# Optimization experiments

Measured on AMD Instinct MI355X. Metric: run time of the kernel, lower is better.

Reference implementation:

```python
import jax, jax.numpy as jnp
import numpy as np

K = 3
STRIDE = 1
PAD = 1
DIL = 1


def _conv2d(x, w, b, stride, pad):
    y = jax.lax.conv_general_dilated(
        x, w, (stride, stride), [(pad, pad), (pad, pad)],
        dimension_numbers=('NCHW', 'OIHW', 'NCHW'))
    return y + b[None, :, None, None]


def setup_inputs() -> dict:
    key = jax.random.key(0)
    ks = jax.random.split(key, 6)
    N, Cin, Cout, H, W = 4, 64, 64, 128, 128
    x = jax.random.normal(ks[0], (N, Cin, H, W), jnp.float32)
    w_off = jax.random.normal(ks[1], (2 * K * K, Cin, K, K), jnp.float32) * 0.01
    b_off = jnp.zeros((2 * K * K,), jnp.float32)
    w_mask = jax.random.normal(ks[2], (K * K, Cin, K, K), jnp.float32) * 0.01
    b_mask = jnp.zeros((K * K,), jnp.float32)
    weight = jax.random.normal(ks[3], (Cout, Cin, K, K), jnp.float32) * 0.05
    bias = jax.random.normal(ks[4], (Cout,), jnp.float32)
    return {"x": x, "w_off": w_off, "b_off": b_off,
            "w_mask": w_mask, "b_mask": b_mask,
            "weight": weight, "bias": bias}


def _deform_conv(x, offset, weight, bias):
    # x: [N,C,H,W]; offset: [N,2*K2,Ho,Wo] with channel layout (dy,dx) per kernel pt
    N, C, H, W = x.shape
    K2 = K * K
    Ho, Wo = offset.shape[2], offset.shape[3]
    off_y = offset[:, 0::2]  # [N,K2,Ho,Wo]
    off_x = offset[:, 1::2]
    ki = jnp.arange(K2) // K
    kj = jnp.arange(K2) % K
    base_y = (jnp.arange(Ho) * STRIDE - PAD)[None, :, None] + (ki * DIL)[:, None, None]
    base_x = (jnp.arange(Wo) * STRIDE - PAD)[None, None, :] + (kj * DIL)[:, None, None]
    py = base_y[None].astype(off_y.dtype) + off_y  # [N,K2,Ho,Wo]
    px = base_x[None].astype(off_x.dtype) + off_x
    y0 = jnp.floor(py)
    x0 = jnp.floor(px)
    wy = py - y0
    wx = px - x0
    xf = x.reshape(N, C, H * W)

    def corner(yi, xi):
        valid = (yi >= 0) & (yi <= H - 1) & (xi >= 0) & (xi <= W - 1)
        yc = jnp.clip(yi, 0, H - 1).astype(jnp.int32)
        xc = jnp.clip(xi, 0, W - 1).astype(jnp.int32)
        idx = (yc * W + xc).reshape(N, -1)  # [N, K2*Ho*Wo]
        g = jnp.take_along_axis(xf, idx[:, None, :], axis=2)  # [N,C,K2*Ho*Wo]
        g = g.reshape(N, C, K2, Ho, Wo)
        return g * valid[:, None].astype(x.dtype)

    # bilinear interpolation with zero padding outside the image
    val = ((1 - wy) * (1 - wx))[:, None] * corner(y0, x0) \
        + ((1 - wy) * wx)[:, None] * corner(y0, x0 + 1) \
        + (wy * (1 - wx))[:, None] * corner(y0 + 1, x0) \
        + (wy * wx)[:, None] * corner(y0 + 1, x0 + 1)  # [N,C,K2,Ho,Wo]
    out = jnp.einsum('nckhw,ock->nohw', val,
                     weight.reshape(weight.shape[0], C, K2))
    return out + bias[None, :, None, None]


def reference(x, w_off, b_off, w_mask, b_mask, weight, bias):
    offset = _conv2d(x, w_off, b_off, STRIDE, PAD)              # [N,2*K2,Ho,Wo]
    mask = jax.nn.sigmoid(_conv2d(x, w_mask, b_mask, STRIDE, PAD))  # [N,K2,Ho,Wo]
    # source does mask.repeat(1,2,1,1) then offset*mask, then plain deform_conv2d
    offset = offset * jnp.concatenate([mask, mask], axis=1)
    return _deform_conv(x, offset, weight, bias)
```

## Files before the change

kernel.cpp:

```cpp
#include <hip/hip_runtime.h>
#include <math.h>

#define HD 128
#define WD 128
#define WP 130
#define CIN 64
#define COUT 64
#define NB 4
#define K2 9
#define HW (HD*WD)
#define CK 576
#define TP 32
#define TPF 16
#define NKK 18

#define WAM   (4 * NKK * 64 * 8)
#define WAO   (2 * NKK * 64 * 8)
#define XTP   ((size_t)NB * WP * WP * CIN)
#define OFFSZ ((size_t)NB * K2 * HW)
#define WTSZ  ((size_t)CK * COUT)

#define PRE_T 1024
#define PRE_H 65
#define PRE_P ((WAM + WAO) / 256)
#define HALO_PER_N 33024
#define HALO_W8 16512

typedef __attribute__((ext_vector_type(8))) short short8;
typedef __attribute__((ext_vector_type(4))) float f32x4;
typedef _Float16 half8 __attribute__((ext_vector_type(8)));
typedef _Float16 half2v __attribute__((ext_vector_type(2)));

__device__ inline unsigned short f2bf(float v) {
    unsigned int u = __float_as_uint(v);
    unsigned int r = u + 0x7fffu + ((u >> 16) & 1u);
    return (unsigned short)(r >> 16);
}
__device__ inline short f2h(float v) {
    _Float16 h = (_Float16)v;
    short s; __builtin_memcpy(&s, &h, 2); return s;
}
__device__ inline unsigned int pack_f16(float a, float b) {
    auto h = __builtin_amdgcn_cvt_pkrtz(a, b);
    unsigned int u; __builtin_memcpy(&u, &h, 4); return u;
}
__device__ inline half2v dup_h2(float a) {
    auto h = __builtin_amdgcn_cvt_pkrtz(a, a);
    half2v r; __builtin_memcpy(&r, &h, 4); return r;
}

__global__ __launch_bounds__(256) void pre_kernel(
    const float* __restrict__ x,
    const float* __restrict__ weight,
    const float* __restrict__ w_off,
    const float* __restrict__ w_mask,
    unsigned short* __restrict__ xp,
    short* __restrict__ mhi, short* __restrict__ ohi)
{
    __shared__ float tile[64][66];
    int bid = blockIdx.x;
    int t = threadIdx.x;

    if (bid < PRE_T) {
        int half = bid & 1;
        int h = (bid >> 1) & 127;
        int n = bid >> 8;
        int w0 = half * 64;
        int g = t >> 6, wl = t & 63;
        const float* xb = x + ((size_t)n * CIN) * HW + h * WD + w0;
        #pragma unroll
        for (int i = 0; i < 16; i++) {
            int cc = i * 4 + g;
            tile[wl][cc] = xb[(size_t)cc * HW + wl];
        }
        __syncthreads();
        size_t rowbase = (((size_t)n * WP + (h + 1)) * WP + (w0 + 1)) * CIN;
        #pragma unroll
        for (int i = 0; i < 8; i++) {
            int u = i * 256 + t;
            int ww = u >> 5;
            int cp = (u & 31) * 2;
            float2 v = *(const float2*)&tile[ww][cp];
            *(unsigned int*)&xp[rowbase + (size_t)ww * CIN + cp] = pack_f16(v.x, v.y);
        }
    } else if (bid < PRE_T + PRE_H) {
        int widx = (bid - PRE_T) * 256 + t;
        if (widx < HALO_W8) {
            int s = widx * 8;
            int n = s / HALO_PER_N;
            int v = s - n * HALO_PER_N;
            size_t nb = (size_t)n * WP * WP * CIN;
            size_t base;
            if (v < 8320) {
                base = nb + v;
            } else if (v < 16640) {
                base = nb + (size_t)129 * WP * CIN + (v - 8320);
            } else if (v < 24832) {
                int v2 = v - 16640; int h = 1 + (v2 >> 6); int c = v2 & 63;
                base = nb + (size_t)h * WP * CIN + c;
            } else {
                int v3 = v - 24832; int h = 1 + (v3 >> 6); int c = v3 & 63;
                base = nb + ((size_t)h * WP + 129) * CIN + c;
            }
            short8 z = {0, 0, 0, 0, 0, 0, 0, 0};
            *(short8*)&xp[base] = z;
        }
    } else {
        int gid = (bid - PRE_T - PRE_H) * 256 + t;
        if (gid < WAM) {
            int idx = gid;
            int jj = idx & 7;
            int lane = (idx >> 3) & 63;
            int kk = (idx >> 9) % NKK;
            int mt = (idx >> 9) / NKK;
            int o = mt * 16 + (lane & 15);
            int rp = kk * 32 + (lane >> 4) * 8 + jj;
            int k = rp >> 6, c = rp & 63;
            mhi[idx] = f2h(weight[((size_t)o * CIN + c) * 9 + k]);
        } else {
            int idx = gid - WAM;
            int jj = idx & 7;
            int lane = (idx >> 3) & 63;
            int kk = (idx >> 9) % NKK;
            int mt = (idx >> 9) / NKK;
            int j = mt * 16 + (lane & 15);
            int rp = kk * 32 + (lane >> 4) * 8 + jj;
            int k = rp >> 6, c = rp & 63;
            float w = 0.f;
            if (j < 18)      w = w_off[((size_t)j * CIN + c) * 9 + k];
            else if (j < 27) w = w_mask[((size_t)(j - 18) * CIN + c) * 9 + k];
            ohi[idx] = f2h(w);
        }
    }
}

__global__ __launch_bounds__(256, 4) void fused_kernel(
    const unsigned short* __restrict__ xp,
    const short* __restrict__ waM_hi,
    const short* __restrict__ waO_hi,
    const float* __restrict__ b_off, const float* __restrict__ b_mask,
    const float* __restrict__ bias,
    float* __restrict__ out)
{
    __shared__ __align__(16) short val_s[72 * 256];
    __shared__ __align__(16) float U[27 * 32];

    int t = threadIdx.x;
    int wv = t >> 6;
    int lane = t & 63;
    int wo0 = blockIdx.x * TP;
    int ho  = blockIdx.y;
    int n   = blockIdx.z;
    const unsigned short* xpn = xp + (size_t)n * WP * WP * CIN;
    int p16 = lane & 15, quad = lane >> 4;

    half8 apre[6];
    #pragma unroll
    for (int kk = 0; kk < 6; kk++)
        apre[kk] = *(const half8*)&waM_hi[((wv * NKK + kk) * 64 + lane) * 8];

    #pragma unroll
    for (int i = 0; i < 9; i++) {
        int u = t + 256 * i;
        int tap = u >> 8;
        int p = (u >> 3) & 31;
        int g = u & 7;
        int ti = tap / 3, tj = tap - ti * 3;
        const short8 v = *(const short8*)&xpn[((size_t)(ho + ti) * WP + (wo0 + p + tj)) * CIN + g * 8];
        int c2 = tap * 8 + g;
        *(short8*)&val_s[c2 * 256 + ((p + c2) & 31) * 8] = v;
    }
    __syncthreads();

    if (wv < 2) {
        int jt = wv;
        f32x4 c0a = {0.f, 0.f, 0.f, 0.f};
        f32x4 c1a = {0.f, 0.f, 0.f, 0.f};
        #pragma unroll
        for (int kk = 0; kk < NKK; kk++) {
            int abase = ((jt * NKK + kk) * 64 + lane) * 8;
            half8 ah = *(const half8*)&waO_hi[abase];
            int c2 = kk * 4 + quad;
            half8 b0 = *(const half8*)&val_s[c2 * 256 + ((p16 + c2) & 31) * 8];
            half8 b1 = *(const half8*)&val_s[c2 * 256 + ((16 + p16 + c2) & 31) * 8];
            c0a = __builtin_amdgcn_mfma_f32_16x16x32_f16(ah, b0, c0a, 0, 0, 0);
            c1a = __builtin_amdgcn_mfma_f32_16x16x32_f16(ah, b1, c1a, 0, 0, 0);
        }
        #pragma unroll
        for (int i = 0; i < 4; i++) {
            int j = jt * 16 + quad * 4 + i;
            if (j < 27) {
                float bv = (j < 18) ? b_off[j] : b_mask[j - 18];
                U[j * 32 + p16] = c0a[i] + bv;
                U[j * 32 + 16 + p16] = c1a[i] + bv;
            }
        }
    }
    __syncthreads();

    float rwy[2], rwx[2];
    unsigned int rmeta[2];
    #pragma unroll
    for (int pass = 0; pass < 2; pass++) {
        int u = t + pass * 256;
        if (u < K2 * TP) {
            int k = u >> 5, p = u & 31;
            float oy_raw = U[(2 * k) * 32 + p];
            float ox_raw = U[(2 * k + 1) * 32 + p];
            float my = 1.f / (1.f + expf(-U[(18 + (2 * k) % 9) * 32 + p]));
            float mx = 1.f / (1.f + expf(-U[(18 + (2 * k + 1) % 9) * 32 + p]));
            float oy = oy_raw * my;
            float ox = ox_raw * mx;
            int ki = k / 3, kj = k - ki * 3;
            int wo = wo0 + p;
            float py = (float)(ho - 1 + ki) + oy;
            float px = (float)(wo - 1 + kj) + ox;
            float y0f = floorf(py), x0f = floorf(px);
            float wy = py - y0f, wx = px - x0f;
            int y0 = (int)y0f, x0 = (int)x0f;
            int y0c = min(max(y0, 0), HD - 1);
            int y1c = min(max(y0 + 1, 0), HD - 1);
            int x0c = min(max(x0, 0), WD - 1);
            int x1c = min(max(x0 + 1, 0), WD - 1);
            bool vy0 = (y0 >= 0) && (y0 < HD);
            bool vy1 = (y0 + 1 >= 0) && (y0 + 1 < HD);
            bool vx0 = (x0 >= 0) && (x0 < WD);
            bool vx1 = (x0 + 1 >= 0) && (x0 + 1 < WD);
            unsigned int cvA = (vy0 && vx0) ? 1u : 0u;
            unsigned int cvB = (vy0 && vx1) ? 1u : 0u;
            unsigned int cvC = (vy1 && vx0) ? 1u : 0u;
            unsigned int cvD = (vy1 && vx1) ? 1u : 0u;
            rwy[pass] = wy;
            rwx[pass] = wx;
            rmeta[pass] = (unsigned int)y0c | ((unsigned int)x0c << 7)
                        | ((unsigned int)(y1c - y0c) << 14) | ((unsigned int)(x1c - x0c) << 15)
                        | (cvA << 16) | (cvB << 17) | (cvC << 18) | (cvD << 19);
        }
    }
    __syncthreads();
    #pragma unroll
    for (int pass = 0; pass < 2; pass++) {
        int u = t + pass * 256;
        if (u < K2 * TP) {
            U[u] = rwy[pass];
            U[288 + u] = rwx[pass];
            ((unsigned int*)U)[576 + u] = rmeta[pass];
        }
    }
    __syncthreads();

    #pragma unroll
    for (int i = 0; i < 9; i++) {
        int u = t + 256 * i;
        int task = u >> 3;
        int g = u & 7;
        int c0 = g * 8;
        int k = task >> 5, p = task & 31;
        float wy = U[task];
        float wx = U[288 + task];
        unsigned int m = ((const unsigned int*)U)[576 + task];
        float wy0 = 1.f - wy, wx0 = 1.f - wx;
        float wA = (m & 0x10000u) ? wy0 * wx0 : 0.f;
        float wB = (m & 0x20000u) ? wy0 * wx  : 0.f;
        float wC = (m & 0x40000u) ? wy  * wx0 : 0.f;
        float wD = (m & 0x80000u) ? wy  * wx  : 0.f;
        half2v wa2 = dup_h2(wA), wb2 = dup_h2(wB), wc2 = dup_h2(wC), wd2 = dup_h2(wD);
        int y0c = (int)(m & 127u);
        int x0c = (int)((m >> 7) & 127u);
        int ry0 = (y0c + 1) * (WP * CIN);
        int ry1 = ry0 + (int)((m >> 14) & 1u) * (WP * CIN);
        int cx0 = (x0c + 1) * CIN + c0;
        int cx1 = (x0c + 1) * CIN + (int)((m >> 15) & 1u) * CIN + c0;
        uint4 qa = *(const uint4*)&xpn[ry0 + cx0];
        uint4 qb = *(const uint4*)&xpn[ry0 + cx1];
        uint4 qc = *(const uint4*)&xpn[ry1 + cx0];
        uint4 qd = *(const uint4*)&xpn[ry1 + cx1];
        unsigned int qa_[4] = {qa.x, qa.y, qa.z, qa.w};
        unsigned int qb_[4] = {qb.x, qb.y, qb.z, qb.w};
        unsigned int qc_[4] = {qc.x, qc.y, qc.z, qc.w};
        unsigned int qd_[4] = {qd.x, qd.y, qd.z, qd.w};
        unsigned int r_[4];
        #pragma unroll
        for (int d = 0; d < 4; d++) {
            half2v ha, hb, hc, hd;
            __builtin_memcpy(&ha, &qa_[d], 4);
            __builtin_memcpy(&hb, &qb_[d], 4);
            __builtin_memcpy(&hc, &qc_[d], 4);
            __builtin_memcpy(&hd, &qd_[d], 4);
            half2v gg = wa2 * ha + wb2 * hb + wc2 * hc + wd2 * hd;
            __builtin_memcpy(&r_[d], &gg, 4);
        }
        uint4 r = {r_[0], r_[1], r_[2], r_[3]};
        int c2 = k * 8 + g;
        *(uint4*)&val_s[c2 * 256 + ((p + c2) & 31) * 8] = r;
    }
    __syncthreads();

    f32x4 a0 = {0.f, 0.f, 0.f, 0.f};
    f32x4 a1 = {0.f, 0.f, 0.f, 0.f};
    #pragma unroll
    for (int kk = 0; kk < NKK; kk++) {
        half8 ah;
        if (kk < 6) ah = apre[kk];
        else        ah = *(const half8*)&waM_hi[((wv * NKK + kk) * 64 + lane) * 8];
        int c2 = kk * 4 + quad;
        half8 b0 = *(const half8*)&val_s[c2 * 256 + ((p16 + c2) & 31) * 8];
        half8 b1 = *(const half8*)&val_s[c2 * 256 + ((16 + p16 + c2) & 31) * 8];
        a0 = __builtin_amdgcn_mfma_f32_16x16x32_f16(ah, b0, a0, 0, 0, 0);
        a1 = __builtin_amdgcn_mfma_f32_16x16x32_f16(ah, b1, a1, 0, 0, 0);
    }

    size_t obase = ((size_t)n * COUT) * HW + (size_t)ho * WD + wo0;
    #pragma unroll
    for (int i = 0; i < 4; i++) {
        int o = wv * 16 + quad * 4 + i;
        float bv = bias[o];
        out[obase + (size_t)o * HW + p16] = a0[i] + bv;
        out[obase + (size_t)o * HW + 16 + p16] = a1[i] + bv;
    }
}

__global__ void transpose_w_kernel(const float* __restrict__ w, float* __restrict__ wt) {
    int i = blockIdx.x * 256 + threadIdx.x;
    int o = i / CK;
    int ck = i - o * CK;
    wt[ck * COUT + o] = w[i];
}

__global__ __launch_bounds__(256) void offmask_kernel(
    const float* __restrict__ x,
    const float* __restrict__ w_off, const float* __restrict__ b_off,
    const float* __restrict__ w_mask, const float* __restrict__ b_mask,
    float* __restrict__ offy, float* __restrict__ offx)
{
    __shared__ float ws[CK][27];
    int t = threadIdx.x;
    for (int i = t; i < CK * 27; i += 256) {
        int j = i % 27;
        int citap = i / 27;
        int ci = citap / 9;
        int tap = citap - ci * 9;
        float v;
        if (j < 18) v = w_off[(j * CIN + ci) * 9 + tap];
        else        v = w_mask[((j - 18) * CIN + ci) * 9 + tap];
        ws[citap][j] = v;
    }
    __syncthreads();

    int pix = blockIdx.x * 256 + t;
    int n  = pix >> 14;
    int ho = (pix >> 7) & 127;
    int wo = pix & 127;

    float acc[27];
    #pragma unroll
    for (int j = 0; j < 18; j++) acc[j] = b_off[j];
    #pragma unroll
    for (int j = 0; j < 9; j++)  acc[18 + j] = b_mask[j];

    int offs[9];
    bool oks[9];
    #pragma unroll
    for (int dy = 0; dy < 3; dy++) {
        int y = ho - 1 + dy;
        #pragma unroll
        for (int dx = 0; dx < 3; dx++) {
            int xx = wo - 1 + dx;
            bool ok = (y >= 0) && (y < HD) && (xx >= 0) && (xx < WD);
            oks[dy * 3 + dx] = ok;
            offs[dy * 3 + dx] = (ok ? y : 0) * WD + (ok ? xx : 0);
        }
    }
    const float* xn = x + (size_t)n * CIN * HW;
    for (int ci = 0; ci < CIN; ci++) {
        const float* xc = xn + (size_t)ci * HW;
        float v[9];
        #pragma unroll
        for (int tap = 0; tap < 9; tap++)
            v[tap] = oks[tap] ? xc[offs[tap]] : 0.f;
        #pragma unroll
        for (int tap = 0; tap < 9; tap++) {
            const float* wrow = ws[ci * 9 + tap];
            float vv = v[tap];
            #pragma unroll
            for (int j = 0; j < 27; j++) acc[j] += wrow[j] * vv;
        }
    }
    float m[9];
    #pragma unroll
    for (int j = 0; j < 9; j++) m[j] = 1.f / (1.f + expf(-acc[18 + j]));
    #pragma unroll
    for (int k = 0; k < 9; k++) {
        int cy = 2 * k, cx = 2 * k + 1;
        float my = m[cy < 9 ? cy : cy - 9];
        float mx = m[cx < 9 ? cx : cx - 9];
        size_t o = (((size_t)n * K2 + k) * HD + ho) * WD + wo;
        offy[o] = acc[cy] * my;
        offx[o] = acc[cx] * mx;
    }
}

__global__ __launch_bounds__(256) void deform_kernel(
    const float* __restrict__ x,
    const float* __restrict__ offy, const float* __restrict__ offx,
    const float* __restrict__ wt,
    const float* __restrict__ bias,
    float* __restrict__ out)
{
    __shared__ __align__(16) float val_f[CK * TPF];
    __shared__ float4 p_w4[K2 * TPF];
    __shared__ int4   p_idx4[K2 * TPF];

    int t = threadIdx.x;
    int wo0 = blockIdx.x * TPF;
    int ho  = blockIdx.y;
    int n   = blockIdx.z;

    if (t < K2 * TPF) {
        int k = t >> 4, p = t & 15;
        int wo = wo0 + p;
        size_t oi = (((size_t)n * K2 + k) * HD + ho) * WD + wo;
        float oy = offy[oi], ox = offx[oi];
        int ki = k / 3, kj = k - ki * 3;
        float py = (float)(ho - 1 + ki) + oy;
        float px = (float)(wo - 1 + kj) + ox;
        float y0f = floorf(py), x0f = floorf(px);
        float wy = py - y0f, wx = px - x0f;
        int y0 = (int)y0f, x0 = (int)x0f;
        float wy0 = 1.f - wy, wx0 = 1.f - wx;
        int y0c = min(max(y0, 0), HD - 1);
        int y1c = min(max(y0 + 1, 0), HD - 1);
        int x0c = min(max(x0, 0), WD - 1);
        int x1c = min(max(x0 + 1, 0), WD - 1);
        bool vy0 = (y0 >= 0) && (y0 < HD);
        bool vy1 = (y0 + 1 >= 0) && (y0 + 1 < HD);
        bool vx0 = (x0 >= 0) && (x0 < WD);
        bool vx1 = (x0 + 1 >= 0) && (x0 + 1 < WD);
        float4 w4;
        w4.x = (vy0 && vx0) ? wy0 * wx0 : 0.f;
        w4.y = (vy0 && vx1) ? wy0 * wx  : 0.f;
        w4.z = (vy1 && vx0) ? wy  * wx0 : 0.f;
        w4.w = (vy1 && vx1) ? wy  * wx  : 0.f;
        int4 i4;
        i4.x = y0c * WD + x0c;
        i4.y = y0c * WD + x1c;
        i4.z = y1c * WD + x0c;
        i4.w = y1c * WD + x1c;
        p_w4[t] = w4;
        p_idx4[t] = i4;
    }
    __syncthreads();

    const float* xn = x + (size_t)n * CIN * HW;
    for (int e = t; e < CK * TPF; e += 256) {
        int row = e >> 4, p = e & 15;
        int cc = row / 9, k = row - cc * 9;
        int task = (k << 4) | p;
        float4 w4 = p_w4[task];
        int4  i4 = p_idx4[task];
        const float* xc = xn + (size_t)cc * HW;
        val_f[e] = w4.x * xc[i4.x] + w4.y * xc[i4.y]
                 + w4.z * xc[i4.z] + w4.w * xc[i4.w];
    }
    __syncthreads();

    int o = t & 63, q = t >> 6;
    float4 acc = {0.f, 0.f, 0.f, 0.f};
    const float4* v4 = (const float4*)val_f;
    const float* wp = wt + o;
    #pragma unroll 4
    for (int r = 0; r < CK; r++) {
        float w = wp[r * COUT];
        float4 vv = v4[r * 4 + q];
        acc.x += w * vv.x; acc.y += w * vv.y;
        acc.z += w * vv.z; acc.w += w * vv.w;
    }
    float b = bias[o];
    acc.x += b; acc.y += b; acc.z += b; acc.w += b;
    __syncthreads();
    float4* o4 = (float4*)val_f;
    o4[o * 4 + q] = acc;
    __syncthreads();
    size_t obase = ((size_t)n * COUT) * HW + (size_t)ho * WD + wo0;
    #pragma unroll
    for (int i = 0; i < 4; i++) {
        int l = t + 256 * i;
        int oo = l >> 4, p = l & 15;
        out[obase + (size_t)oo * HW + p] = val_f[l];
    }
}

extern "C" void kernel_launch(void* const* d_in, const int* in_sizes, int n_in,
                              void* d_out, int out_size, void* d_ws, size_t ws_size,
                              hipStream_t stream) {
    const float* x      = (const float*)d_in[0];
    const float* w_off  = (const float*)d_in[1];
    const float* b_off  = (const float*)d_in[2];
    const float* w_mask = (const float*)d_in[3];
    const float* b_mask = (const float*)d_in[4];
    const float* weight = (const float*)d_in[5];
    const float* bias   = (const float*)d_in[6];
    float* out = (float*)d_out;

    short* base = (short*)d_ws;
    short* waM_hi = base;
    short* waO_hi = waM_hi + WAM;
    unsigned short* xp = (unsigned short*)(waO_hi + WAO);
    size_t need = ((size_t)WAM + WAO + XTP) * sizeof(short);

    if (ws_size >= need) {
        pre_kernel<<<PRE_T + PRE_H + PRE_P, 256, 0, stream>>>(
            x, weight, w_off, w_mask, xp, waM_hi, waO_hi);
        fused_kernel<<<dim3(WD / TP, HD, NB), 256, 0, stream>>>(
            xp, waM_hi, waO_hi, b_off, b_mask, bias, out);
    } else {
        float* offy = (float*)d_ws;
        float* offx = offy + OFFSZ;
        float* wt   = offx + OFFSZ;
        transpose_w_kernel<<<144, 256, 0, stream>>>(weight, wt);
        offmask_kernel<<<256, 256, 0, stream>>>(x, w_off, b_off, w_mask, b_mask, offy, offx);
        deform_kernel<<<dim3(WD / TPF, HD, NB), 256, 0, stream>>>(x, offy, offx, wt, bias, out);
    }
}
```

Baseline: 107.9 us.

## Compute sampling metadata in registers and distribute via wave shuffles

```diff
diff --git a/kernel.cpp b/kernel.cpp
--- a/kernel.cpp
+++ b/kernel.cpp
@@ -13,6 +13,7 @@
 #define TP 32
 #define TPF 16
 #define NKK 18
+#define US 33
 
 #define WAM   (4 * NKK * 64 * 8)
 #define WAO   (2 * NKK * 64 * 8)
@@ -134,6 +135,35 @@
     }
 }
 
+#define CALC_TRIPLE(kk_, owy, owx, ometa) { \
+    const int k_ = (kk_); \
+    float oy_raw = U[(2 * k_) * US + p]; \
+    float ox_raw = U[(2 * k_ + 1) * US + p]; \
+    float my = 1.f / (1.f + expf(-U[(18 + (2 * k_) % 9) * US + p])); \
+    float mx = 1.f / (1.f + expf(-U[(18 + (2 * k_ + 1) % 9) * US + p])); \
+    float oy = oy_raw * my; \
+    float ox = ox_raw * mx; \
+    const int ki_ = k_ / 3, kj_ = k_ - ki_ * 3; \
+    float py = (float)(ho - 1 + ki_) + oy; \
+    float px = (float)(wo0 + p - 1 + kj_) + ox; \
+    float y0f = floorf(py), x0f = floorf(px); \
+    float wy_ = py - y0f, wx_ = px - x0f; \
+    int y0 = (int)y0f, x0 = (int)x0f; \
+    int y0c = min(max(y0, 0), HD - 1); \
+    int y1c = min(max(y0 + 1, 0), HD - 1); \
+    int x0c = min(max(x0, 0), WD - 1); \
+    int x1c = min(max(x0 + 1, 0), WD - 1); \
+    bool vy0 = (y0 >= 0) && (y0 < HD); \
+    bool vy1 = (y0 + 1 >= 0) && (y0 + 1 < HD); \
+    bool vx0 = (x0 >= 0) && (x0 < WD); \
+    bool vx1 = (x0 + 1 >= 0) && (x0 + 1 < WD); \
+    owy = wy_; owx = wx_; \
+    ometa = (unsigned int)y0c | ((unsigned int)x0c << 7) \
+          | ((unsigned int)(y1c - y0c) << 14) | ((unsigned int)(x1c - x0c) << 15) \
+          | ((vy0 && vx0) ? 0x10000u : 0u) | ((vy0 && vx1) ? 0x20000u : 0u) \
+          | ((vy1 && vx0) ? 0x40000u : 0u) | ((vy1 && vx1) ? 0x80000u : 0u); \
+}
+
 __global__ __launch_bounds__(256, 4) void fused_kernel(
     const unsigned short* __restrict__ xp,
     const short* __restrict__ waM_hi,
@@ -143,7 +173,7 @@
     float* __restrict__ out)
 {
     __shared__ __align__(16) short val_s[72 * 256];
-    __shared__ __align__(16) float U[27 * 32];
+    __shared__ __align__(16) float U[27 * US];
 
     int t = threadIdx.x;
     int wv = t >> 6;
@@ -191,108 +221,66 @@
             int j = jt * 16 + quad * 4 + i;
             if (j < 27) {
                 float bv = (j < 18) ? b_off[j] : b_mask[j - 18];
-                U[j * 32 + p16] = c0a[i] + bv;
-                U[j * 32 + 16 + p16] = c1a[i] + bv;
+                U[j * US + p16] = c0a[i] + bv;
+                U[j * US + 16 + p16] = c1a[i] + bv;
             }
         }
     }
     __syncthreads();
 
-    float rwy[2], rwx[2];
-    unsigned int rmeta[2];
-    #pragma unroll
-    for (int pass = 0; pass < 2; pass++) {
-        int u = t + pass * 256;
-        if (u < K2 * TP) {
-            int k = u >> 5, p = u & 31;
-            float oy_raw = U[(2 * k) * 32 + p];
-            float ox_raw = U[(2 * k + 1) * 32 + p];
-            float my = 1.f / (1.f + expf(-U[(18 + (2 * k) % 9) * 32 + p]));
-            float mx = 1.f / (1.f + expf(-U[(18 + (2 * k + 1) % 9) * 32 + p]));
-            float oy = oy_raw * my;
-            float ox = ox_raw * mx;
-            int ki = k / 3, kj = k - ki * 3;
-            int wo = wo0 + p;
-            float py = (float)(ho - 1 + ki) + oy;
-            float px = (float)(wo - 1 + kj) + ox;
-            float y0f = floorf(py), x0f = floorf(px);
-            float wy = py - y0f, wx = px - x0f;
-            int y0 = (int)y0f, x0 = (int)x0f;
-            int y0c = min(max(y0, 0), HD - 1);
-            int y1c = min(max(y0 + 1, 0), HD - 1);
-            int x0c = min(max(x0, 0), WD - 1);
-            int x1c = min(max(x0 + 1, 0), WD - 1);
-            bool vy0 = (y0 >= 0) && (y0 < HD);
-            bool vy1 = (y0 + 1 >= 0) && (y0 + 1 < HD);
-            bool vx0 = (x0 >= 0) && (x0 < WD);
-            bool vx1 = (x0 + 1 >= 0) && (x0 + 1 < WD);
-            unsigned int cvA = (vy0 && vx0) ? 1u : 0u;
-            unsigned int cvB = (vy0 && vx1) ? 1u : 0u;
-            unsigned int cvC = (vy1 && vx0) ? 1u : 0u;
-            unsigned int cvD = (vy1 && vx1) ? 1u : 0u;
-            rwy[pass] = wy;
-            rwx[pass] = wx;
-            rmeta[pass] = (unsigned int)y0c | ((unsigned int)x0c << 7)
-                        | ((unsigned int)(y1c - y0c) << 14) | ((unsigned int)(x1c - x0c) << 15)
-                        | (cvA << 16) | (cvB << 17) | (cvC << 18) | (cvD << 19);
-        }
-    }
-    __syncthreads();
-    #pragma unroll
-    for (int pass = 0; pass < 2; pass++) {
-        int u = t + pass * 256;
-        if (u < K2 * TP) {
-            U[u] = rwy[pass];
-            U[288 + u] = rwx[pass];
-            ((unsigned int*)U)[576 + u] = rmeta[pass];
-        }
-    }
-    __syncthreads();
-
-    #pragma unroll
-    for (int i = 0; i < 9; i++) {
-        int u = t + 256 * i;
-        int task = u >> 3;
-        int g = u & 7;
-        int c0 = g * 8;
-        int k = task >> 5, p = task & 31;
-        float wy = U[task];
-        float wx = U[288 + task];
-        unsigned int m = ((const unsigned int*)U)[576 + task];
-        float wy0 = 1.f - wy, wx0 = 1.f - wx;
-        float wA = (m & 0x10000u) ? wy0 * wx0 : 0.f;
-        float wB = (m & 0x20000u) ? wy0 * wx  : 0.f;
-        float wC = (m & 0x40000u) ? wy  * wx0 : 0.f;
-        float wD = (m & 0x80000u) ? wy  * wx  : 0.f;
-        half2v wa2 = dup_h2(wA), wb2 = dup_h2(wB), wc2 = dup_h2(wC), wd2 = dup_h2(wD);
-        int y0c = (int)(m & 127u);
-        int x0c = (int)((m >> 7) & 127u);
-        int ry0 = (y0c + 1) * (WP * CIN);
-        int ry1 = ry0 + (int)((m >> 14) & 1u) * (WP * CIN);
-        int cx0 = (x0c + 1) * CIN + c0;
-        int cx1 = (x0c + 1) * CIN + (int)((m >> 15) & 1u) * CIN + c0;
-        uint4 qa = *(const uint4*)&xpn[ry0 + cx0];
-        uint4 qb = *(const uint4*)&xpn[ry0 + cx1];
-        uint4 qc = *(const uint4*)&xpn[ry1 + cx0];
-        uint4 qd = *(const uint4*)&xpn[ry1 + cx1];
-        unsigned int qa_[4] = {qa.x, qa.y, qa.z, qa.w};
-        unsigned int qb_[4] = {qb.x, qb.y, qb.z, qb.w};
-        unsigned int qc_[4] = {qc.x, qc.y, qc.z, qc.w};
-        unsigned int qd_[4] = {qd.x, qd.y, qd.z, qd.w};
-        unsigned int r_[4];
-        #pragma unroll
-        for (int d = 0; d < 4; d++) {
-            half2v ha, hb, hc, hd;
-            __builtin_memcpy(&ha, &qa_[d], 4);
-            __builtin_memcpy(&hb, &qb_[d], 4);
-            __builtin_memcpy(&hc, &qc_[d], 4);
-            __builtin_memcpy(&hd, &qd_[d], 4);
-            half2v gg = wa2 * ha + wb2 * hb + wc2 * hc + wd2 * hd;
-            __builtin_memcpy(&r_[d], &gg, 4);
-        }
-        uint4 r = {r_[0], r_[1], r_[2], r_[3]};
-        int c2 = k * 8 + g;
-        *(uint4*)&val_s[c2 * 256 + ((p + c2) & 31) * 8] = r;
+    {
+        int p = t >> 3, g = t & 7, c0 = g * 8;
+        float myWy, myWx; unsigned int myMeta;
+        CALC_TRIPLE(g, myWy, myWx, myMeta);
+        float w8y, w8x; unsigned int m8;
+        CALC_TRIPLE(8, w8y, w8x, m8);
+
+        #pragma unroll
+        for (int k = 0; k < 9; k++) {
+            float wy, wx; unsigned int m;
+            if (k < 8) {
+                int sl = (lane & 56) | k;
+                wy = __shfl(myWy, sl);
+                wx = __shfl(myWx, sl);
+                m  = (unsigned int)__shfl((int)myMeta, sl);
+            } else {
+                wy = w8y; wx = w8x; m = m8;
+            }
+            float wy0 = 1.f - wy, wx0 = 1.f - wx;
+            float wA = (m & 0x10000u) ? wy0 * wx0 : 0.f;
+            float wB = (m & 0x20000u) ? wy0 * wx  : 0.f;
+            float wC = (m & 0x40000u) ? wy  * wx0 : 0.f;
+            float wD = (m & 0x80000u) ? wy  * wx  : 0.f;
+            half2v wa2 = dup_h2(wA), wb2 = dup_h2(wB), wc2 = dup_h2(wC), wd2 = dup_h2(wD);
+            int y0c = (int)(m & 127u);
+            int x0c = (int)((m >> 7) & 127u);
+            int ry0 = (y0c + 1) * (WP * CIN);
+            int ry1 = ry0 + (int)((m >> 14) & 1u) * (WP * CIN);
+            int cx0 = (x0c + 1) * CIN + c0;
+            int cx1 = (x0c + 1) * CIN + (int)((m >> 15) & 1u) * CIN + c0;
+            uint4 qa = *(const uint4*)&xpn[ry0 + cx0];
+            uint4 qb = *(const uint4*)&xpn[ry0 + cx1];
+            uint4 qc = *(const uint4*)&xpn[ry1 + cx0];
+            uint4 qd = *(const uint4*)&xpn[ry1 + cx1];
+            unsigned int qa_[4] = {qa.x, qa.y, qa.z, qa.w};
+            unsigned int qb_[4] = {qb.x, qb.y, qb.z, qb.w};
+            unsigned int qc_[4] = {qc.x, qc.y, qc.z, qc.w};
+            unsigned int qd_[4] = {qd.x, qd.y, qd.z, qd.w};
+            unsigned int r_[4];
+            #pragma unroll
+            for (int d = 0; d < 4; d++) {
+                half2v ha, hb, hc, hd;
+                __builtin_memcpy(&ha, &qa_[d], 4);
+                __builtin_memcpy(&hb, &qb_[d], 4);
+                __builtin_memcpy(&hc, &qc_[d], 4);
+                __builtin_memcpy(&hd, &qd_[d], 4);
+                half2v gg = wa2 * ha + wb2 * hb + wc2 * hc + wd2 * hd;
+                __builtin_memcpy(&r_[d], &gg, 4);
+            }
+            uint4 r = {r_[0], r_[1], r_[2], r_[3]};
+            int c2 = k * 8 + g;
+            *(uint4*)&val_s[c2 * 256 + ((p + c2) & 31) * 8] = r;
+        }
     }
     __syncthreads();
 
```

Result: slower. 124.8 us (+15.6%).

## Move offset/mask conv into pre-kernel, pass bilinear metadata through workspace

Applied to the files above, without the earlier changes.

```diff
diff --git a/kernel.cpp b/kernel.cpp
--- a/kernel.cpp
+++ b/kernel.cpp
@@ -15,14 +15,14 @@
 #define NKK 18
 
 #define WAM   (4 * NKK * 64 * 8)
-#define WAO   (2 * NKK * 64 * 8)
 #define XTP   ((size_t)NB * WP * WP * CIN)
 #define OFFSZ ((size_t)NB * K2 * HW)
 #define WTSZ  ((size_t)CK * COUT)
 
 #define PRE_T 1024
 #define PRE_H 65
-#define PRE_P ((WAM + WAO) / 256)
+#define PRE_W 144
+#define PRE_C 256
 #define HALO_PER_N 33024
 #define HALO_W8 16512
 
@@ -31,11 +31,6 @@
 typedef _Float16 half8 __attribute__((ext_vector_type(8)));
 typedef _Float16 half2v __attribute__((ext_vector_type(2)));
 
-__device__ inline unsigned short f2bf(float v) {
-    unsigned int u = __float_as_uint(v);
-    unsigned int r = u + 0x7fffu + ((u >> 16) & 1u);
-    return (unsigned short)(r >> 16);
-}
 __device__ inline short f2h(float v) {
     _Float16 h = (_Float16)v;
     short s; __builtin_memcpy(&s, &h, 2); return s;
@@ -52,16 +47,19 @@
 __global__ __launch_bounds__(256) void pre_kernel(
     const float* __restrict__ x,
     const float* __restrict__ weight,
-    const float* __restrict__ w_off,
-    const float* __restrict__ w_mask,
+    const float* __restrict__ w_off, const float* __restrict__ b_off,
+    const float* __restrict__ w_mask, const float* __restrict__ b_mask,
     unsigned short* __restrict__ xp,
-    short* __restrict__ mhi, short* __restrict__ ohi)
+    short* __restrict__ mhi,
+    float* __restrict__ wyP, float* __restrict__ wxP,
+    unsigned int* __restrict__ metaP)
 {
-    __shared__ float tile[64][66];
+    __shared__ __align__(16) unsigned char smem[32256];
     int bid = blockIdx.x;
     int t = threadIdx.x;
 
     if (bid < PRE_T) {
+        float (*tile)[66] = (float (*)[66])smem;
         int half = bid & 1;
         int h = (bid >> 1) & 127;
         int n = bid >> 8;
@@ -105,114 +103,99 @@
             short8 z = {0, 0, 0, 0, 0, 0, 0, 0};
             *(short8*)&xp[base] = z;
         }
+    } else if (bid < PRE_T + PRE_H + PRE_W) {
+        int idx = (bid - PRE_T - PRE_H) * 256 + t;
+        int jj = idx & 7;
+        int lane = (idx >> 3) & 63;
+        int kk = (idx >> 9) % NKK;
+        int mt = (idx >> 9) / NKK;
+        int o = mt * 16 + (lane & 15);
+        int rp = kk * 32 + (lane >> 4) * 8 + jj;
+        int k = rp >> 6, c = rp & 63;
+        mhi[idx] = f2h(weight[((size_t)o * CIN + c) * 9 + k]);
     } else {
-        int gid = (bid - PRE_T - PRE_H) * 256 + t;
-        if (gid < WAM) {
-            int idx = gid;
-            int jj = idx & 7;
-            int lane = (idx >> 3) & 63;
-            int kk = (idx >> 9) % NKK;
-            int mt = (idx >> 9) / NKK;
-            int o = mt * 16 + (lane & 15);
-            int rp = kk * 32 + (lane >> 4) * 8 + jj;
-            int k = rp >> 6, c = rp & 63;
-            mhi[idx] = f2h(weight[((size_t)o * CIN + c) * 9 + k]);
-        } else {
-            int idx = gid - WAM;
-            int jj = idx & 7;
-            int lane = (idx >> 3) & 63;
-            int kk = (idx >> 9) % NKK;
-            int mt = (idx >> 9) / NKK;
-            int j = mt * 16 + (lane & 15);
-            int rp = kk * 32 + (lane >> 4) * 8 + jj;
-            int k = rp >> 6, c = rp & 63;
-            float w = 0.f;
-            if (j < 18)      w = w_off[((size_t)j * CIN + c) * 9 + k];
-            else if (j < 27) w = w_mask[((size_t)(j - 18) * CIN + c) * 9 + k];
-            ohi[idx] = f2h(w);
-        }
-    }
-}
-
-__global__ __launch_bounds__(256, 4) void fused_kernel(
-    const unsigned short* __restrict__ xp,
-    const short* __restrict__ waM_hi,
-    const short* __restrict__ waO_hi,
-    const float* __restrict__ b_off, const float* __restrict__ b_mask,
-    const float* __restrict__ bias,
-    float* __restrict__ out)
-{
-    __shared__ __align__(16) short val_s[72 * 256];
-    __shared__ __align__(16) float U[27 * 32];
-
-    int t = threadIdx.x;
-    int wv = t >> 6;
-    int lane = t & 63;
-    int wo0 = blockIdx.x * TP;
-    int ho  = blockIdx.y;
-    int n   = blockIdx.z;
-    const unsigned short* xpn = xp + (size_t)n * WP * WP * CIN;
-    int p16 = lane & 15, quad = lane >> 4;
-
-    half8 apre[6];
-    #pragma unroll
-    for (int kk = 0; kk < 6; kk++)
-        apre[kk] = *(const half8*)&waM_hi[((wv * NKK + kk) * 64 + lane) * 8];
-
-    #pragma unroll
-    for (int i = 0; i < 9; i++) {
-        int u = t + 256 * i;
-        int tap = u >> 8;
-        int p = (u >> 3) & 31;
-        int g = u & 7;
-        int ti = tap / 3, tj = tap - ti * 3;
-        const short8 v = *(const short8*)&xpn[((size_t)(ho + ti) * WP + (wo0 + p + tj)) * CIN + g * 8];
-        int c2 = tap * 8 + g;
-        *(short8*)&val_s[c2 * 256 + ((p + c2) & 31) * 8] = v;
-    }
-    __syncthreads();
-
-    if (wv < 2) {
-        int jt = wv;
-        f32x4 c0a = {0.f, 0.f, 0.f, 0.f};
-        f32x4 c1a = {0.f, 0.f, 0.f, 0.f};
-        #pragma unroll
-        for (int kk = 0; kk < NKK; kk++) {
-            int abase = ((jt * NKK + kk) * 64 + lane) * 8;
-            half8 ah = *(const half8*)&waO_hi[abase];
-            int c2 = kk * 4 + quad;
-            half8 b0 = *(const half8*)&val_s[c2 * 256 + ((p16 + c2) & 31) * 8];
-            half8 b1 = *(const half8*)&val_s[c2 * 256 + ((16 + p16 + c2) & 31) * 8];
-            c0a = __builtin_amdgcn_mfma_f32_16x16x32_f16(ah, b0, c0a, 0, 0, 0);
-            c1a = __builtin_amdgcn_mfma_f32_16x16x32_f16(ah, b1, c1a, 0, 0, 0);
-        }
-        #pragma unroll
-        for (int i = 0; i < 4; i++) {
-            int j = jt * 16 + quad * 4 + i;
-            if (j < 27) {
-                float bv = (j < 18) ? b_off[j] : b_mask[j - 18];
-                U[j * 32 + p16] = c0a[i] + bv;
-                U[j * 32 + 16 + p16] = c1a[i] + bv;
+        unsigned int (*wsH)[14] = (unsigned int (*)[14])smem;
+        for (int e = t; e < CK * 14; e += 256) {
+            int m = e % 14;
+            int citap = e / 14;
+            int ci = citap / 9, tap = citap - ci * 9;
+            int j0 = 2 * m, j1 = 2 * m + 1;
+            float w0 = (j0 < 18) ? w_off[((size_t)j0 * CIN + ci) * 9 + tap]
+                                 : w_mask[((size_t)(j0 - 18) * CIN + ci) * 9 + tap];
+            float w1;
+            if (j1 < 18)      w1 = w_off[((size_t)j1 * CIN + ci) * 9 + tap];
+            else if (j1 < 27) w1 = w_mask[((size_t)(j1 - 18) * CIN + ci) * 9 + tap];
+            else              w1 = 0.f;
+            wsH[citap][m] = pack_f16(w0, w1);
+        }
+        __syncthreads();
+
+        int pix = (bid - (PRE_T + PRE_H + PRE_W)) * 256 + t;
+        int n  = pix >> 14;
+        int ho = (pix >> 7) & 127;
+        int wo = pix & 127;
+
+        int offs[9];
+        bool oks[9];
+        #pragma unroll
+        for (int dy = 0; dy < 3; dy++) {
+            int y = ho - 1 + dy;
+            #pragma unroll
+            for (int dx = 0; dx < 3; dx++) {
+                int xx = wo - 1 + dx;
+                bool ok = (y >= 0) && (y < HD) && (xx >= 0) && (xx < WD);
+                oks[dy * 3 + dx] = ok;
+                offs[dy * 3 + dx] = (ok ? y : 0) * WD + (ok ? xx : 0);
             }
         }
-    }
-    __syncthreads();
-
-    float rwy[2], rwx[2];
-    unsigned int rmeta[2];
-    #pragma unroll
-    for (int pass = 0; pass < 2; pass++) {
-        int u = t + pass * 256;
-        if (u < K2 * TP) {
-            int k = u >> 5, p = u & 31;
-            float oy_raw = U[(2 * k) * 32 + p];
-            float ox_raw = U[(2 * k + 1) * 32 + p];
-            float my = 1.f / (1.f + expf(-U[(18 + (2 * k) % 9) * 32 + p]));
-            float mx = 1.f / (1.f + expf(-U[(18 + (2 * k + 1) % 9) * 32 + p]));
-            float oy = oy_raw * my;
-            float ox = ox_raw * mx;
+
+        float accf[27];
+        #pragma unroll
+        for (int j = 0; j < 27; j++) accf[j] = 0.f;
+
+        const float* xn = x + (size_t)n * CIN * HW;
+        #pragma unroll 1
+        for (int cc = 0; cc < 4; cc++) {
+            half2v acc2[14];
+            #pragma unroll
+            for (int m = 0; m < 14; m++) acc2[m] = (half2v)(_Float16)0.f;
+            for (int ci = cc * 16; ci < cc * 16 + 16; ci++) {
+                const float* xc = xn + (size_t)ci * HW;
+                float v[9];
+                #pragma unroll
+                for (int tap = 0; tap < 9; tap++)
+                    v[tap] = oks[tap] ? xc[offs[tap]] : 0.f;
+                #pragma unroll
+                for (int tap = 0; tap < 9; tap++) {
+                    half2v vh = dup_h2(v[tap]);
+                    const unsigned int* wrow = wsH[ci * 9 + tap];
+                    #pragma unroll
+                    for (int m = 0; m < 14; m++) {
+                        half2v w; __builtin_memcpy(&w, &wrow[m], 4);
+                        acc2[m] = vh * w + acc2[m];
+                    }
+                }
+            }
+            #pragma unroll
+            for (int m = 0; m < 14; m++) {
+                accf[2 * m] += (float)acc2[m][0];
+                if (2 * m + 1 < 27) accf[2 * m + 1] += (float)acc2[m][1];
+            }
+        }
+        #pragma unroll
+        for (int j = 0; j < 18; j++) accf[j] += b_off[j];
+        #pragma unroll
+        for (int j = 0; j < 9; j++)  accf[18 + j] += b_mask[j];
+
+        float mk[9];
+        #pragma unroll
+        for (int j = 0; j < 9; j++) mk[j] = 1.f / (1.f + expf(-accf[18 + j]));
+
+        #pragma unroll
+        for (int k = 0; k < 9; k++) {
+            float oy = accf[2 * k] * mk[(2 * k) % 9];
+            float ox = accf[2 * k + 1] * mk[(2 * k + 1) % 9];
             int ki = k / 3, kj = k - ki * 3;
-            int wo = wo0 + p;
             float py = (float)(ho - 1 + ki) + oy;
             float px = (float)(wo - 1 + kj) + ox;
             float y0f = floorf(py), x0f = floorf(px);
@@ -226,73 +209,86 @@
             bool vy1 = (y0 + 1 >= 0) && (y0 + 1 < HD);
             bool vx0 = (x0 >= 0) && (x0 < WD);
             bool vx1 = (x0 + 1 >= 0) && (x0 + 1 < WD);
-            unsigned int cvA = (vy0 && vx0) ? 1u : 0u;
-            unsigned int cvB = (vy0 && vx1) ? 1u : 0u;
-            unsigned int cvC = (vy1 && vx0) ? 1u : 0u;
-            unsigned int cvD = (vy1 && vx1) ? 1u : 0u;
-            rwy[pass] = wy;
-            rwx[pass] = wx;
-            rmeta[pass] = (unsigned int)y0c | ((unsigned int)x0c << 7)
-                        | ((unsigned int)(y1c - y0c) << 14) | ((unsigned int)(x1c - x0c) << 15)
-                        | (cvA << 16) | (cvB << 17) | (cvC << 18) | (cvD << 19);
-        }
-    }
-    __syncthreads();
-    #pragma unroll
-    for (int pass = 0; pass < 2; pass++) {
-        int u = t + pass * 256;
-        if (u < K2 * TP) {
-            U[u] = rwy[pass];
-            U[288 + u] = rwx[pass];
-            ((unsigned int*)U)[576 + u] = rmeta[pass];
-        }
-    }
-    __syncthreads();
-
-    #pragma unroll
-    for (int i = 0; i < 9; i++) {
-        int u = t + 256 * i;
-        int task = u >> 3;
-        int g = u & 7;
-        int c0 = g * 8;
-        int k = task >> 5, p = task & 31;
-        float wy = U[task];
-        float wx = U[288 + task];
-        unsigned int m = ((const unsigned int*)U)[576 + task];
-        float wy0 = 1.f - wy, wx0 = 1.f - wx;
-        float wA = (m & 0x10000u) ? wy0 * wx0 : 0.f;
-        float wB = (m & 0x20000u) ? wy0 * wx  : 0.f;
-        float wC = (m & 0x40000u) ? wy  * wx0 : 0.f;
-        float wD = (m & 0x80000u) ? wy  * wx  : 0.f;
-        half2v wa2 = dup_h2(wA), wb2 = dup_h2(wB), wc2 = dup_h2(wC), wd2 = dup_h2(wD);
-        int y0c = (int)(m & 127u);
-        int x0c = (int)((m >> 7) & 127u);
-        int ry0 = (y0c + 1) * (WP * CIN);
-        int ry1 = ry0 + (int)((m >> 14) & 1u) * (WP * CIN);
-        int cx0 = (x0c + 1) * CIN + c0;
-        int cx1 = (x0c + 1) * CIN + (int)((m >> 15) & 1u) * CIN + c0;
-        uint4 qa = *(const uint4*)&xpn[ry0 + cx0];
-        uint4 qb = *(const uint4*)&xpn[ry0 + cx1];
-        uint4 qc = *(const uint4*)&xpn[ry1 + cx0];
-        uint4 qd = *(const uint4*)&xpn[ry1 + cx1];
-        unsigned int qa_[4] = {qa.x, qa.y, qa.z, qa.w};
-        unsigned int qb_[4] = {qb.x, qb.y, qb.z, qb.w};
-        unsigned int qc_[4] = {qc.x, qc.y, qc.z, qc.w};
-        unsigned int qd_[4] = {qd.x, qd.y, qd.z, qd.w};
-        unsigned int r_[4];
-        #pragma unroll
-        for (int d = 0; d < 4; d++) {
-            half2v ha, hb, hc, hd;
-            __builtin_memcpy(&ha, &qa_[d], 4);
-            __builtin_memcpy(&hb, &qb_[d], 4);
-            __builtin_memcpy(&hc, &qc_[d], 4);
-            __builtin_memcpy(&hd, &qd_[d], 4);
-            half2v gg = wa2 * ha + wb2 * hb + wc2 * hc + wd2 * hd;
-            __builtin_memcpy(&r_[d], &gg, 4);
-        }
-        uint4 r = {r_[0], r_[1], r_[2], r_[3]};
-        int c2 = k * 8 + g;
-        *(uint4*)&val_s[c2 * 256 + ((p + c2) & 31) * 8] = r;
+            unsigned int meta = (unsigned int)y0c | ((unsigned int)x0c << 7)
+                | ((unsigned int)(y1c - y0c) << 14) | ((unsigned int)(x1c - x0c) << 15)
+                | ((vy0 && vx0) ? 0x10000u : 0u) | ((vy0 && vx1) ? 0x20000u : 0u)
+                | ((vy1 && vx0) ? 0x40000u : 0u) | ((vy1 && vx1) ? 0x80000u : 0u);
+            size_t pi = (size_t)(n * K2 + k) * HW + ho * WD + wo;
+            wyP[pi] = wy;
+            wxP[pi] = wx;
+            metaP[pi] = meta;
+        }
+    }
+}
+
+__global__ __launch_bounds__(256, 4) void fused_kernel(
+    const unsigned short* __restrict__ xp,
+    const short* __restrict__ waM_hi,
+    const float* __restrict__ wyP, const float* __restrict__ wxP,
+    const unsigned int* __restrict__ metaP,
+    const float* __restrict__ bias,
+    float* __restrict__ out)
+{
+    __shared__ __align__(16) short val_s[72 * 256];
+
+    int t = threadIdx.x;
+    int wv = t >> 6;
+    int lane = t & 63;
+    int wo0 = blockIdx.x * TP;
+    int ho  = blockIdx.y;
+    int n   = blockIdx.z;
+    const unsigned short* xpn = xp + (size_t)n * WP * WP * CIN;
+    int p16 = lane & 15, quad = lane >> 4;
+
+    half8 apre[8];
+    #pragma unroll
+    for (int kk = 0; kk < 8; kk++)
+        apre[kk] = *(const half8*)&waM_hi[((wv * NKK + kk) * 64 + lane) * 8];
+
+    {
+        int p = t >> 3, g = t & 7, c0 = g * 8;
+        size_t pbase = (size_t)(n * K2) * HW + (size_t)ho * WD + wo0 + p;
+        #pragma unroll
+        for (int i = 0; i < 9; i++) {
+            size_t pi = pbase + (size_t)i * HW;
+            float wy = wyP[pi];
+            float wx = wxP[pi];
+            unsigned int m = metaP[pi];
+            float wy0 = 1.f - wy, wx0 = 1.f - wx;
+            float wA = (m & 0x10000u) ? wy0 * wx0 : 0.f;
+            float wB = (m & 0x20000u) ? wy0 * wx  : 0.f;
+            float wC = (m & 0x40000u) ? wy  * wx0 : 0.f;
+            float wD = (m & 0x80000u) ? wy  * wx  : 0.f;
+            half2v wa2 = dup_h2(wA), wb2 = dup_h2(wB), wc2 = dup_h2(wC), wd2 = dup_h2(wD);
+            int y0c = (int)(m & 127u);
+            int x0c = (int)((m >> 7) & 127u);
+            int ry0 = (y0c + 1) * (WP * CIN);
+            int ry1 = ry0 + (int)((m >> 14) & 1u) * (WP * CIN);
+            int cx0 = (x0c + 1) * CIN + c0;
+            int cx1 = (x0c + 1) * CIN + (int)((m >> 15) & 1u) * CIN + c0;
+            uint4 qa = *(const uint4*)&xpn[ry0 + cx0];
+            uint4 qb = *(const uint4*)&xpn[ry0 + cx1];
+            uint4 qc = *(const uint4*)&xpn[ry1 + cx0];
+            uint4 qd = *(const uint4*)&xpn[ry1 + cx1];
+            unsigned int qa_[4] = {qa.x, qa.y, qa.z, qa.w};
+            unsigned int qb_[4] = {qb.x, qb.y, qb.z, qb.w};
+            unsigned int qc_[4] = {qc.x, qc.y, qc.z, qc.w};
+            unsigned int qd_[4] = {qd.x, qd.y, qd.z, qd.w};
+            unsigned int r_[4];
+            #pragma unroll
+            for (int d = 0; d < 4; d++) {
+                half2v ha, hb, hc, hd;
+                __builtin_memcpy(&ha, &qa_[d], 4);
+                __builtin_memcpy(&hb, &qb_[d], 4);
+                __builtin_memcpy(&hc, &qc_[d], 4);
+                __builtin_memcpy(&hd, &qd_[d], 4);
+                half2v gg = wa2 * ha + wb2 * hb + wc2 * hc + wd2 * hd;
+                __builtin_memcpy(&r_[d], &gg, 4);
+            }
+            uint4 r = {r_[0], r_[1], r_[2], r_[3]};
+            int c2 = i * 8 + g;
+            *(uint4*)&val_s[c2 * 256 + ((p + c2) & 31) * 8] = r;
+        }
     }
     __syncthreads();
 
@@ -301,7 +297,7 @@
     #pragma unroll
     for (int kk = 0; kk < NKK; kk++) {
         half8 ah;
-        if (kk < 6) ah = apre[kk];
+        if (kk < 8) ah = apre[kk];
         else        ah = *(const half8*)&waM_hi[((wv * NKK + kk) * 64 + lane) * 8];
         int c2 = kk * 4 + quad;
         half8 b0 = *(const half8*)&val_s[c2 * 256 + ((p16 + c2) & 31) * 8];
@@ -502,17 +498,18 @@
     const float* bias   = (const float*)d_in[6];
     float* out = (float*)d_out;
 
-    short* base = (short*)d_ws;
-    short* waM_hi = base;
-    short* waO_hi = waM_hi + WAM;
-    unsigned short* xp = (unsigned short*)(waO_hi + WAO);
-    size_t need = ((size_t)WAM + WAO + XTP) * sizeof(short);
+    short* waM_hi = (short*)d_ws;
+    unsigned short* xp = (unsigned short*)(waM_hi + WAM);
+    float* wyP = (float*)(xp + XTP);
+    float* wxP = wyP + OFFSZ;
+    unsigned int* metaP = (unsigned int*)(wxP + OFFSZ);
+    size_t need = (size_t)WAM * 2 + XTP * 2 + OFFSZ * 12;
 
     if (ws_size >= need) {
-        pre_kernel<<<PRE_T + PRE_H + PRE_P, 256, 0, stream>>>(
-            x, weight, w_off, w_mask, xp, waM_hi, waO_hi);
+        pre_kernel<<<PRE_T + PRE_H + PRE_W + PRE_C, 256, 0, stream>>>(
+            x, weight, w_off, b_off, w_mask, b_mask, xp, waM_hi, wyP, wxP, metaP);
         fused_kernel<<<dim3(WD / TP, HD, NB), 256, 0, stream>>>(
-            xp, waM_hi, waO_hi, b_off, b_mask, bias, out);
+            xp, waM_hi, wyP, wxP, metaP, bias, out);
     } else {
         float* offy = (float*)d_ws;
         float* offx = offy + OFFSZ;
```

New measurement: 191.4 us. 1.77x slower.

## Stage padded input window in LDS and gather bilinear corners from it

Applied to the files above, without the earlier changes.

```diff
diff --git a/kernel.cpp b/kernel.cpp
--- a/kernel.cpp
+++ b/kernel.cpp
@@ -13,6 +13,8 @@
 #define TP 32
 #define TPF 16
 #define NKK 18
+#define WR 6
+#define WC 36
 
 #define WAM   (4 * NKK * 64 * 8)
 #define WAO   (2 * NKK * 64 * 8)
@@ -31,11 +33,6 @@
 typedef _Float16 half8 __attribute__((ext_vector_type(8)));
 typedef _Float16 half2v __attribute__((ext_vector_type(2)));
 
-__device__ inline unsigned short f2bf(float v) {
-    unsigned int u = __float_as_uint(v);
-    unsigned int r = u + 0x7fffu + ((u >> 16) & 1u);
-    return (unsigned short)(r >> 16);
-}
 __device__ inline short f2h(float v) {
     _Float16 h = (_Float16)v;
     short s; __builtin_memcpy(&s, &h, 2); return s;
@@ -134,7 +131,9 @@
     }
 }
 
-__global__ __launch_bounds__(256, 4) void fused_kernel(
+#define WIN_ADDR(r, c, g) ((((r) * WC + (c)) * 8 + (((g) + (c)) & 7)) * 8)
+
+__global__ __launch_bounds__(256, 2) void fused_kernel(
     const unsigned short* __restrict__ xp,
     const short* __restrict__ waM_hi,
     const short* __restrict__ waO_hi,
@@ -142,6 +141,7 @@
     const float* __restrict__ bias,
     float* __restrict__ out)
 {
+    __shared__ __align__(16) short win_s[WR * WC * 64];
     __shared__ __align__(16) short val_s[72 * 256];
     __shared__ __align__(16) float U[27 * 32];
 
@@ -160,15 +160,16 @@
         apre[kk] = *(const half8*)&waM_hi[((wv * NKK + kk) * 64 + lane) * 8];
 
     #pragma unroll
-    for (int i = 0; i < 9; i++) {
+    for (int i = 0; i < 7; i++) {
         int u = t + 256 * i;
-        int tap = u >> 8;
-        int p = (u >> 3) & 31;
-        int g = u & 7;
-        int ti = tap / 3, tj = tap - ti * 3;
-        const short8 v = *(const short8*)&xpn[((size_t)(ho + ti) * WP + (wo0 + p + tj)) * CIN + g * 8];
-        int c2 = tap * 8 + g;
-        *(short8*)&val_s[c2 * 256 + ((p + c2) & 31) * 8] = v;
+        if (u < WR * WC * 8) {
+            int s = u >> 3, g = u & 7;
+            int r = s / WC, c = s - r * WC;
+            int yr = min(max(ho - 1 + r, 0), 129);
+            int xc = min(max(wo0 - 1 + c, 0), 129);
+            const short8 v = *(const short8*)&xpn[((size_t)yr * WP + xc) * CIN + g * 8];
+            *(short8*)&win_s[WIN_ADDR(r, c, g)] = v;
+        }
     }
     __syncthreads();
 
@@ -180,9 +181,15 @@
         for (int kk = 0; kk < NKK; kk++) {
             int abase = ((jt * NKK + kk) * 64 + lane) * 8;
             half8 ah = *(const half8*)&waO_hi[abase];
-            int c2 = kk * 4 + quad;
-            half8 b0 = *(const half8*)&val_s[c2 * 256 + ((p16 + c2) & 31) * 8];
-            half8 b1 = *(const half8*)&val_s[c2 * 256 + ((16 + p16 + c2) & 31) * 8];
+            const int tap = kk >> 1;
+            const int ti = tap / 3;
+            const int tj = tap - ti * 3;
+            int gg = (kk & 1) * 4 + quad;
+            int r = ti + 1;
+            int ca = p16 + tj + 1;
+            int cb = 16 + p16 + tj + 1;
+            half8 b0 = *(const half8*)&win_s[WIN_ADDR(r, ca, gg)];
+            half8 b1 = *(const half8*)&win_s[WIN_ADDR(r, cb, gg)];
             c0a = __builtin_amdgcn_mfma_f32_16x16x32_f16(ah, b0, c0a, 0, 0, 0);
             c1a = __builtin_amdgcn_mfma_f32_16x16x32_f16(ah, b1, c1a, 0, 0, 0);
         }
@@ -226,15 +233,15 @@
             bool vy1 = (y0 + 1 >= 0) && (y0 + 1 < HD);
             bool vx0 = (x0 >= 0) && (x0 < WD);
             bool vx1 = (x0 + 1 >= 0) && (x0 + 1 < WD);
-            unsigned int cvA = (vy0 && vx0) ? 1u : 0u;
-            unsigned int cvB = (vy0 && vx1) ? 1u : 0u;
-            unsigned int cvC = (vy1 && vx0) ? 1u : 0u;
-            unsigned int cvD = (vy1 && vx1) ? 1u : 0u;
+            bool inW = (y0c >= ho - 2) && (y1c <= ho + 3)
+                    && (x0c >= wo0 - 2) && (x1c <= wo0 + 33);
             rwy[pass] = wy;
             rwx[pass] = wx;
             rmeta[pass] = (unsigned int)y0c | ((unsigned int)x0c << 7)
                         | ((unsigned int)(y1c - y0c) << 14) | ((unsigned int)(x1c - x0c) << 15)
-                        | (cvA << 16) | (cvB << 17) | (cvC << 18) | (cvD << 19);
+                        | ((vy0 && vx0) ? 0x10000u : 0u) | ((vy0 && vx1) ? 0x20000u : 0u)
+                        | ((vy1 && vx0) ? 0x40000u : 0u) | ((vy1 && vx1) ? 0x80000u : 0u)
+                        | (inW ? 0x100000u : 0u);
         }
     }
     __syncthreads();
@@ -267,14 +274,28 @@
         half2v wa2 = dup_h2(wA), wb2 = dup_h2(wB), wc2 = dup_h2(wC), wd2 = dup_h2(wD);
         int y0c = (int)(m & 127u);
         int x0c = (int)((m >> 7) & 127u);
-        int ry0 = (y0c + 1) * (WP * CIN);
-        int ry1 = ry0 + (int)((m >> 14) & 1u) * (WP * CIN);
-        int cx0 = (x0c + 1) * CIN + c0;
-        int cx1 = (x0c + 1) * CIN + (int)((m >> 15) & 1u) * CIN + c0;
-        uint4 qa = *(const uint4*)&xpn[ry0 + cx0];
-        uint4 qb = *(const uint4*)&xpn[ry0 + cx1];
-        uint4 qc = *(const uint4*)&xpn[ry1 + cx0];
-        uint4 qd = *(const uint4*)&xpn[ry1 + cx1];
+        int dy1 = (int)((m >> 14) & 1u);
+        int dx1 = (int)((m >> 15) & 1u);
+        uint4 qa, qb, qc, qd;
+        if (m & 0x100000u) {
+            int r0 = y0c - (ho - 2);
+            int r1 = r0 + dy1;
+            int cA = x0c - (wo0 - 2);
+            int cB = cA + dx1;
+            qa = *(const uint4*)&win_s[WIN_ADDR(r0, cA, g)];
+            qb = *(const uint4*)&win_s[WIN_ADDR(r0, cB, g)];
+            qc = *(const uint4*)&win_s[WIN_ADDR(r1, cA, g)];
+            qd = *(const uint4*)&win_s[WIN_ADDR(r1, cB, g)];
+        } else {
+            int ry0 = (y0c + 1) * (WP * CIN);
+            int ry1 = ry0 + dy1 * (WP * CIN);
+            int cx0 = (x0c + 1) * CIN + c0;
+            int cx1 = (x0c + 1) * CIN + dx1 * CIN + c0;
+            qa = *(const uint4*)&xpn[ry0 + cx0];
+            qb = *(const uint4*)&xpn[ry0 + cx1];
+            qc = *(const uint4*)&xpn[ry1 + cx0];
+            qd = *(const uint4*)&xpn[ry1 + cx1];
+        }
         unsigned int qa_[4] = {qa.x, qa.y, qa.z, qa.w};
         unsigned int qb_[4] = {qb.x, qb.y, qb.z, qb.w};
         unsigned int qc_[4] = {qc.x, qc.y, qc.z, qc.w};
```

After: 118.3 us. 1.1x slower.
